# Kernel optimization log

Hardware: AMD Instinct MI355X
Metric: run time of the kernel (lower is better)

## Reference

```python
import jax, jax.numpy as jnp
import numpy as np
import math


def _lsq(x, s, bit, all_positive):
    # LSQ fake-quant: scale -> clamp -> round (STE) -> dequant
    if all_positive:
        qn, qp = 0.0, float(2 ** bit - 1)
    else:
        qn, qp = -float(2 ** (bit - 1)), float(2 ** (bit - 1) - 1)
    g = 1.0 / math.sqrt(x.size * qp)  # grad-scale factor (static)
    sg = s * g
    s_eff = sg + jax.lax.stop_gradient(s - sg)  # fwd = s, grad scaled by g
    xq = jnp.clip(x / s_eff, qn, qp)
    xq = xq + jax.lax.stop_gradient(jnp.round(xq) - xq)  # round with STE
    return xq * s_eff


def _conv(x, w, stride):
    return jax.lax.conv_general_dilated(
        x, w, window_strides=(stride, stride), padding='VALID',
        dimension_numbers=('NCHW', 'OIHW', 'NCHW'))


def setup_inputs() -> dict:
    key = jax.random.key(0)
    ks = jax.random.split(key, 5)
    B = 65536
    x = jax.random.normal(ks[0], (B, 1, 28, 28), dtype=jnp.float32)
    w1 = jax.random.normal(ks[1], (4, 1, 5, 5), dtype=jnp.float32) * 0.2
    w2 = jax.random.normal(ks[2], (8, 4, 3, 3), dtype=jnp.float32) * 0.2
    fc_w = jax.random.normal(ks[3], (10, 200), dtype=jnp.float32) * 0.07
    fc_b = jax.random.normal(ks[4], (10,), dtype=jnp.float32) * 0.01
    one = jnp.ones((1,), dtype=jnp.float32)
    return {"x": x, "w1": w1, "w2": w2, "fc_w": fc_w, "fc_b": fc_b,
            "s_in": one * 0.05, "s_w1": one * 0.02, "s_a1": one * 0.05,
            "s_w2": one * 0.02, "s_a2": one * 0.05, "s_fc": one * 0.02}


def reference(x, w1, w2, fc_w, fc_b, s_in, s_w1, s_a1, s_w2, s_a2, s_fc):
    x = _lsq(x, s_in, 8, False)
    x = _conv(x, _lsq(w1, s_w1, 8, False), 2)          # [B,4,12,12]
    x = jax.nn.relu(_lsq(x, s_a1, 8, True))
    x = _conv(x, _lsq(w2, s_w2, 8, False), 2)          # [B,8,5,5]
    x = jax.nn.relu(_lsq(x, s_a2, 8, True))
    x = x.reshape(x.shape[0], -1)                      # [B,200]
    return x @ _lsq(fc_w, s_fc, 8, False).T + fc_b     # [B,10]
```

## Files before the change

### kernel.cpp

```cpp
#include <hip/hip_runtime.h>
#include <math.h>

#define G  8
#define NG 8

#if __has_builtin(__builtin_amdgcn_sdot4)
__device__ __forceinline__ int dot4(unsigned a, unsigned b, int c) {
    return __builtin_amdgcn_sdot4((int)a, (int)b, c, false);
}
#else
__device__ __forceinline__ int dot4(unsigned a, unsigned b, int c) {
    c += (int)(signed char)(a & 255u)         * (int)(signed char)(b & 255u);
    c += (int)(signed char)((a >> 8) & 255u)  * (int)(signed char)((b >> 8) & 255u);
    c += (int)(signed char)((a >> 16) & 255u) * (int)(signed char)((b >> 16) & 255u);
    c += (int)(signed char)(a >> 24)          * (int)(signed char)(b >> 24);
    return c;
}
#endif

__device__ __forceinline__ void wave_fence() {
    asm volatile("s_waitcnt lgkmcnt(0)" ::: "memory");
}

__device__ __forceinline__ float seff(float s, float gf) {
    float sg = s * gf;
    return sg + (s - sg);
}
__device__ __forceinline__ unsigned q8(float v, float s, float rs) {
    float q0 = v * rs;
    float r  = fmaf(-s, q0, v);
    float y  = fmaf(r, rs, q0);
    y = fminf(fmaxf(y, -128.f), 127.f);
    float t = y + 12582912.0f;
    return __float_as_uint(t);
}
__device__ __forceinline__ unsigned pack4(unsigned a, unsigned b, unsigned c, unsigned d) {
    return (a & 255u) | ((b & 255u) << 8) | ((c & 255u) << 16) | (d << 24);
}
__device__ __forceinline__ int mround(int acc, double r) {
    double t = fma((double)acc, r, 6755399441055744.0);
    return (int)__double_as_longlong(t);
}


extern "C" __global__ __launch_bounds__(256, 4)
void qcnn_fused(const float* __restrict__ x,  const float* __restrict__ w1,
                const float* __restrict__ w2, const float* __restrict__ fcw,
                const float* __restrict__ fcb,
                const float* __restrict__ s_in, const float* __restrict__ s_w1,
                const float* __restrict__ s_a1, const float* __restrict__ s_w2,
                const float* __restrict__ s_a2, const float* __restrict__ s_fc,
                float* __restrict__ out, int B,
                float gx, float gw1, float ga1, float gw2, float ga2, float gfc)
{
    __shared__ __align__(16) unsigned xs[2][G*224];
    __shared__ __align__(16) unsigned a1p[2][G*144];
    __shared__ __align__(16) unsigned a2p[2][G*50];
    __shared__ __align__(16) unsigned w1pk[4][5][4];
    __shared__ unsigned w2p[8][9];
    __shared__ unsigned fcp[10][50];
    __shared__ int K2s[8];
    __shared__ int K3s[10];
    __shared__ float fcbs[10];

    const int tid = threadIdx.x;
    const int g   = tid >> 5;
    const int t   = tid & 31;

    const float sx  = seff(s_in[0], gx);
    const float sw1 = seff(s_w1[0], gw1);
    const float sa1 = seff(s_a1[0], ga1);
    const float sw2 = seff(s_w2[0], gw2);
    const float sa2 = seff(s_a2[0], ga2);
    const float sfc = seff(s_fc[0], gfc);
    const float rsx = 1.0f / sx;
    const float rw1 = 1.0f / sw1;
    const float rw2 = 1.0f / sw2;
    const float rfc = 1.0f / sfc;
    const double r1 = (double)sx  * (double)sw1 / (double)sa1;
    const double r2 = (double)sa1 * (double)sw2 / (double)sa2;
    const double r3 = (double)sa2 * (double)sfc;

    const long long gbase = (long long)blockIdx.x * NG;

    const int c8 = t & 7;
    const int eb = (t >> 3) * 7 + c8 - (c8 > 3 ? 1 : 0);

    float4 Rv0, Rv1, Rv2, Rv3, Rv4, Rv5, Rv6;
    auto stage_load = [&](long long grp) {
        const long long img = grp * G + g;
        if (img >= B) return;
        const float4* xp = (const float4*)x + img * 196;
        Rv0 = xp[eb];        Rv1 = xp[eb + 28];  Rv2 = xp[eb + 56];
        Rv3 = xp[eb + 84];   Rv4 = xp[eb + 112]; Rv5 = xp[eb + 140];
        Rv6 = xp[eb + 168];
    };
    auto stage_write = [&](long long grp, int buf) {
        const long long img = grp * G + g;
        if (img >= B) return;
        unsigned* dst = &xs[buf][g*224];
        float4 v;
        v = Rv0; dst[t]       = pack4(q8(v.x,sx,rsx), q8(v.y,sx,rsx), q8(v.z,sx,rsx), q8(v.w,sx,rsx));
        v = Rv1; dst[t + 32]  = pack4(q8(v.x,sx,rsx), q8(v.y,sx,rsx), q8(v.z,sx,rsx), q8(v.w,sx,rsx));
        v = Rv2; dst[t + 64]  = pack4(q8(v.x,sx,rsx), q8(v.y,sx,rsx), q8(v.z,sx,rsx), q8(v.w,sx,rsx));
        v = Rv3; dst[t + 96]  = pack4(q8(v.x,sx,rsx), q8(v.y,sx,rsx), q8(v.z,sx,rsx), q8(v.w,sx,rsx));
        v = Rv4; dst[t + 128] = pack4(q8(v.x,sx,rsx), q8(v.y,sx,rsx), q8(v.z,sx,rsx), q8(v.w,sx,rsx));
        v = Rv5; dst[t + 160] = pack4(q8(v.x,sx,rsx), q8(v.y,sx,rsx), q8(v.z,sx,rsx), q8(v.w,sx,rsx));
        v = Rv6; dst[t + 192] = pack4(q8(v.x,sx,rsx), q8(v.y,sx,rsx), q8(v.z,sx,rsx), q8(v.w,sx,rsx));
    };

    stage_load(gbase);

    if (tid < 80) {
        const int c = tid / 20, rem = tid % 20, ky = rem >> 2, vv = rem & 3;
        const float* wr = w1 + c*25 + ky*5;
        unsigned b[5];
        #pragma unroll
        for (int k = 0; k < 5; ++k) b[k] = q8(wr[k], sw1, rw1) & 255u;
        unsigned pk;
        if      (vv == 0) pk = b[0] | (b[1] << 8) | (b[2] << 16) | (b[3] << 24);
        else if (vv == 1) pk = b[4];
        else if (vv == 2) pk = (b[0] << 16) | (b[1] << 24);
        else              pk = b[2] | (b[3] << 8) | (b[4] << 16);
        w1pk[c][ky][vv] = pk;
    } else if (tid < 152) {
        const int d = tid - 80, oc = d / 9, tap = d % 9;
        unsigned pk = 0;
        #pragma unroll
        for (int ic = 0; ic < 4; ++ic)
            pk |= (q8(w2[oc*36 + ic*9 + tap], sw2, rw2) & 255u) << (8*ic);
        w2p[oc][tap] = pk;
    }
    if (tid < 10) fcbs[tid] = fcb[tid];
    for (int i = tid; i < 500; i += 256) {
        const int o = i / 50, kd = i % 50;
        const float* fr = fcw + o*200 + kd*4;
        fcp[o][kd] = pack4(q8(fr[0],sfc,rfc), q8(fr[1],sfc,rfc),
                           q8(fr[2],sfc,rfc), q8(fr[3],sfc,rfc));
    }
    __syncthreads();
    if (tid < 8) {
        int s = 0;
        #pragma unroll
        for (int d = 0; d < 9; ++d) s = dot4(w2p[tid][d], 0x01010101u, s);
        K2s[tid] = s << 7;
    } else if (tid < 18) {
        const int o = tid - 8;
        int s = 0;
        for (int d = 0; d < 50; ++d) s = dot4(fcp[o][d], 0x01010101u, s);
        K3s[o] = s << 7;
    }
    __syncthreads();
    stage_write(gbase, 0);
    wave_fence();

    for (int it = 0; it < NG + 2; ++it) {
        const long long grp = gbase + it;

        if (it + 1 < NG) stage_load(grp + 1);

        if (it < NG && (grp * G + g) < B) {
            const int c  = t & 3;
            const int h  = (t >> 2) & 1;
            const int y0 = t >> 3;
            uint4 W[5];
            #pragma unroll
            for (int ky = 0; ky < 5; ++ky)
                W[ky] = *(const uint4*)&w1pk[c][ky][0];
            const unsigned* xb = &xs[it & 1][g*224];
            unsigned char* a1b = (unsigned char*)&a1p[it & 1][0];
            #pragma unroll
            for (int k = 0; k < 3; ++k) {
                const int y = y0 + 4*k;
                int acc[6] = {0,0,0,0,0,0};
                #pragma unroll
                for (int ky = 0; ky < 5; ++ky) {
                    const uint4 R = *(const uint4*)&xb[(2*y + ky)*8 + 4*h];
                    acc[0] = dot4(R.y, W[ky].y, dot4(R.x, W[ky].x, acc[0]));
                    acc[1] = dot4(R.y, W[ky].w, dot4(R.x, W[ky].z, acc[1]));
                    acc[2] = dot4(R.z, W[ky].y, dot4(R.y, W[ky].x, acc[2]));
                    acc[3] = dot4(R.z, W[ky].w, dot4(R.y, W[ky].z, acc[3]));
                    acc[4] = dot4(R.w, W[ky].y, dot4(R.z, W[ky].x, acc[4]));
                    acc[5] = dot4(R.w, W[ky].w, dot4(R.z, W[ky].z, acc[5]));
                }
                unsigned char* dst = a1b + (g*144 + y*12 + 6*h)*4 + c;
                #pragma unroll
                for (int m = 0; m < 6; ++m) {
                    int q = mround(acc[m], r1);
                    q = min(max(q, 0), 255);
                    dst[4*m] = (unsigned char)(q - 128);
                }
            }
        }

        if (it >= 1 && it <= NG && ((grp - 1) * G + g) < B) {
            const int oc = t >> 2;
            unsigned wv[9];
            #pragma unroll
            for (int d = 0; d < 9; ++d) wv[d] = w2p[oc][d];
            const int k2 = K2s[oc];
            const unsigned* base = &a1p[(it - 1) & 1][g*144];
            unsigned char* dstb = (unsigned char*)&a2p[(it - 1) & 1][0] + g*200 + oc*25;
            #pragma unroll
            for (int pass = 0; pass < 2; ++pass) {
                const int y = pass ? 4 : (t & 3);
                if (pass && (t & 3) != 0) break;
                unsigned rw[3][12];
                #pragma unroll
                for (int ky = 0; ky < 3; ++ky) {
                    const uint4* rp = (const uint4*)&base[(2*y + ky)*12];
                    uint4 A = rp[0], Bv = rp[1], Cv = rp[2];
                    rw[ky][0]=A.x;  rw[ky][1]=A.y;  rw[ky][2]=A.z;  rw[ky][3]=A.w;
                    rw[ky][4]=Bv.x; rw[ky][5]=Bv.y; rw[ky][6]=Bv.z; rw[ky][7]=Bv.w;
                    rw[ky][8]=Cv.x; rw[ky][9]=Cv.y; rw[ky][10]=Cv.z; rw[ky][11]=Cv.w;
                }
                #pragma unroll
                for (int jx = 0; jx < 5; ++jx) {
                    int acc = k2;
                    #pragma unroll
                    for (int ky = 0; ky < 3; ++ky)
                        #pragma unroll
                        for (int kx = 0; kx < 3; ++kx)
                            acc = dot4(rw[ky][2*jx + kx], wv[ky*3 + kx], acc);
                    int q = mround(acc, r2);
                    q = min(max(q, 0), 255);
                    dstb[y*5 + jx] = (unsigned char)(q - 128);
                }
            }
        }

        if (it >= 2 && ((grp - 2) * G + g) < B && t < 30) {
            const int part = t / 10;
            const int o    = t - part*10;
            const int k0   = part * 17;
            const int nk   = (part == 2) ? 16 : 17;
            const unsigned* a2b = &a2p[it & 1][g*50];
            int acc = 0;
            for (int ki = 0; ki < nk; ++ki) {
                const int k = k0 + ki;
                acc = dot4(a2b[k], fcp[o][k], acc);
            }
            const int self0 = (g & 1) * 32 + o;
            const int s1 = __shfl(acc, self0 + 10);
            const int s2 = __shfl(acc, self0 + 20);
            if (part == 0) {
                const int total = acc + s1 + s2 + K3s[o];
                const double oo = (double)total * r3 + (double)fcbs[o];
                out[((grp - 2)*G + g)*10 + o] = (float)oo;
            }
        }

        if (it + 1 < NG) stage_write(grp + 1, (it + 1) & 1);

        wave_fence();
    }
}

extern "C" void kernel_launch(void* const* d_in, const int* in_sizes, int n_in,
                              void* d_out, int out_size, void* d_ws, size_t ws_size,
                              hipStream_t stream) {
    const float* x    = (const float*)d_in[0];
    const float* w1   = (const float*)d_in[1];
    const float* w2   = (const float*)d_in[2];
    const float* fcw  = (const float*)d_in[3];
    const float* fcb  = (const float*)d_in[4];
    const float* s_in = (const float*)d_in[5];
    const float* s_w1 = (const float*)d_in[6];
    const float* s_a1 = (const float*)d_in[7];
    const float* s_w2 = (const float*)d_in[8];
    const float* s_a2 = (const float*)d_in[9];
    const float* s_fc = (const float*)d_in[10];

    const int B = in_sizes[0] / 784;
    const float gx  = (float)(1.0 / sqrt((double)B * 784.0 * 127.0));
    const float gw1 = (float)(1.0 / sqrt(100.0 * 127.0));
    const float ga1 = (float)(1.0 / sqrt((double)B * 576.0 * 255.0));
    const float gw2 = (float)(1.0 / sqrt(288.0 * 127.0));
    const float ga2 = (float)(1.0 / sqrt((double)B * 200.0 * 255.0));
    const float gfc = (float)(1.0 / sqrt(2000.0 * 127.0));

    const int imgs_per_block = G * NG;
    const int grid = (B + imgs_per_block - 1) / imgs_per_block;
    qcnn_fused<<<grid, 256, 0, stream>>>(x, w1, w2, fcw, fcb,
                                         s_in, s_w1, s_a1, s_w2, s_a2, s_fc,
                                         (float*)d_out, B,
                                         gx, gw1, ga1, gw2, ga2, gfc);
}
```

Before: 55.53 us.

## Reorganize input LDS layout for row reuse in conv1 and vectorize FC dot

The quantized input tile is stored in LDS with a new row-strided layout (stride 72 per 4-row band), so each thread computes three consecutive conv1 output rows and reuses each loaded input row across overlapping kernel windows instead of reloading it per output row. The FC stage pads activations and weights to 52 words so it can use 16-byte vector LDS loads with a fixed unrolled trip count. The cost is a larger LDS footprint for the input buffer, plus more live accumulator registers in conv1, which may reduce occupancy.

```diff
diff --git a/kernel.cpp b/kernel.cpp
--- a/kernel.cpp
+++ b/kernel.cpp
@@ -53,12 +53,12 @@
                 float* __restrict__ out, int B,
                 float gx, float gw1, float ga1, float gw2, float ga2, float gfc)
 {
-    __shared__ __align__(16) unsigned xs[2][G*224];
+    __shared__ __align__(16) unsigned xs[2][G*336];
     __shared__ __align__(16) unsigned a1p[2][G*144];
-    __shared__ __align__(16) unsigned a2p[2][G*50];
+    __shared__ __align__(16) unsigned a2p[2][G*52];
     __shared__ __align__(16) unsigned w1pk[4][5][4];
     __shared__ unsigned w2p[8][9];
-    __shared__ unsigned fcp[10][50];
+    __shared__ __align__(16) unsigned fcp[10][52];
     __shared__ int K2s[8];
     __shared__ int K3s[10];
     __shared__ float fcbs[10];
@@ -85,6 +85,7 @@
 
     const int c8 = t & 7;
     const int eb = (t >> 3) * 7 + c8 - (c8 > 3 ? 1 : 0);
+    const int db = (t >> 3) * 12 + c8;
 
     float4 Rv0, Rv1, Rv2, Rv3, Rv4, Rv5, Rv6;
     auto stage_load = [&](long long grp) {
@@ -98,15 +99,15 @@
     auto stage_write = [&](long long grp, int buf) {
         const long long img = grp * G + g;
         if (img >= B) return;
-        unsigned* dst = &xs[buf][g*224];
+        unsigned* dst = &xs[buf][g*336];
         float4 v;
-        v = Rv0; dst[t]       = pack4(q8(v.x,sx,rsx), q8(v.y,sx,rsx), q8(v.z,sx,rsx), q8(v.w,sx,rsx));
-        v = Rv1; dst[t + 32]  = pack4(q8(v.x,sx,rsx), q8(v.y,sx,rsx), q8(v.z,sx,rsx), q8(v.w,sx,rsx));
-        v = Rv2; dst[t + 64]  = pack4(q8(v.x,sx,rsx), q8(v.y,sx,rsx), q8(v.z,sx,rsx), q8(v.w,sx,rsx));
-        v = Rv3; dst[t + 96]  = pack4(q8(v.x,sx,rsx), q8(v.y,sx,rsx), q8(v.z,sx,rsx), q8(v.w,sx,rsx));
-        v = Rv4; dst[t + 128] = pack4(q8(v.x,sx,rsx), q8(v.y,sx,rsx), q8(v.z,sx,rsx), q8(v.w,sx,rsx));
-        v = Rv5; dst[t + 160] = pack4(q8(v.x,sx,rsx), q8(v.y,sx,rsx), q8(v.z,sx,rsx), q8(v.w,sx,rsx));
-        v = Rv6; dst[t + 192] = pack4(q8(v.x,sx,rsx), q8(v.y,sx,rsx), q8(v.z,sx,rsx), q8(v.w,sx,rsx));
+        v = Rv0; dst[db]       = pack4(q8(v.x,sx,rsx), q8(v.y,sx,rsx), q8(v.z,sx,rsx), q8(v.w,sx,rsx));
+        v = Rv1; dst[db + 48]  = pack4(q8(v.x,sx,rsx), q8(v.y,sx,rsx), q8(v.z,sx,rsx), q8(v.w,sx,rsx));
+        v = Rv2; dst[db + 96]  = pack4(q8(v.x,sx,rsx), q8(v.y,sx,rsx), q8(v.z,sx,rsx), q8(v.w,sx,rsx));
+        v = Rv3; dst[db + 144] = pack4(q8(v.x,sx,rsx), q8(v.y,sx,rsx), q8(v.z,sx,rsx), q8(v.w,sx,rsx));
+        v = Rv4; dst[db + 192] = pack4(q8(v.x,sx,rsx), q8(v.y,sx,rsx), q8(v.z,sx,rsx), q8(v.w,sx,rsx));
+        v = Rv5; dst[db + 240] = pack4(q8(v.x,sx,rsx), q8(v.y,sx,rsx), q8(v.z,sx,rsx), q8(v.w,sx,rsx));
+        v = Rv6; dst[db + 288] = pack4(q8(v.x,sx,rsx), q8(v.y,sx,rsx), q8(v.z,sx,rsx), q8(v.w,sx,rsx));
     };
 
     stage_load(gbase);
@@ -167,30 +168,40 @@
             #pragma unroll
             for (int ky = 0; ky < 5; ++ky)
                 W[ky] = *(const uint4*)&w1pk[c][ky][0];
-            const unsigned* xb = &xs[it & 1][g*224];
+            const unsigned* xb = &xs[it & 1][g*336 + y0*72 + 4*h];
             unsigned char* a1b = (unsigned char*)&a1p[it & 1][0];
-            #pragma unroll
-            for (int k = 0; k < 3; ++k) {
-                const int y = y0 + 4*k;
-                int acc[6] = {0,0,0,0,0,0};
-                #pragma unroll
-                for (int ky = 0; ky < 5; ++ky) {
-                    const uint4 R = *(const uint4*)&xb[(2*y + ky)*8 + 4*h];
-                    acc[0] = dot4(R.y, W[ky].y, dot4(R.x, W[ky].x, acc[0]));
-                    acc[1] = dot4(R.y, W[ky].w, dot4(R.x, W[ky].z, acc[1]));
-                    acc[2] = dot4(R.z, W[ky].y, dot4(R.y, W[ky].x, acc[2]));
-                    acc[3] = dot4(R.z, W[ky].w, dot4(R.y, W[ky].z, acc[3]));
-                    acc[4] = dot4(R.w, W[ky].y, dot4(R.z, W[ky].x, acc[4]));
-                    acc[5] = dot4(R.w, W[ky].w, dot4(R.z, W[ky].z, acc[5]));
-                }
-                unsigned char* dst = a1b + (g*144 + y*12 + 6*h)*4 + c;
-                #pragma unroll
-                for (int m = 0; m < 6; ++m) {
-                    int q = mround(acc[m], r1);
-                    q = min(max(q, 0), 255);
-                    dst[4*m] = (unsigned char)(q - 128);
-                }
-            }
+            int aA[6] = {0,0,0,0,0,0};
+            int aB[6] = {0,0,0,0,0,0};
+            int aC[6] = {0,0,0,0,0,0};
+#define APPLY(A, Wk, R) \
+            A[0] = dot4(R.y, Wk.y, dot4(R.x, Wk.x, A[0])); \
+            A[1] = dot4(R.y, Wk.w, dot4(R.x, Wk.z, A[1])); \
+            A[2] = dot4(R.z, Wk.y, dot4(R.y, Wk.x, A[2])); \
+            A[3] = dot4(R.z, Wk.w, dot4(R.y, Wk.z, A[3])); \
+            A[4] = dot4(R.w, Wk.y, dot4(R.z, Wk.x, A[4])); \
+            A[5] = dot4(R.w, Wk.w, dot4(R.z, Wk.z, A[5]))
+#define EPI(A, yy) { \
+            unsigned char* dst = a1b + (g*144 + (yy)*12 + 6*h)*4 + c; \
+            _Pragma("unroll") \
+            for (int m = 0; m < 6; ++m) { \
+                int q = mround(A[m], r1); \
+                q = min(max(q, 0), 255); \
+                dst[4*m] = (unsigned char)(q - 128); } }
+            uint4 R;
+            R = *(const uint4*)&xb[0];   APPLY(aA, W[0], R);
+            R = *(const uint4*)&xb[12];  APPLY(aA, W[1], R);
+            R = *(const uint4*)&xb[24];  APPLY(aA, W[2], R); APPLY(aB, W[0], R);
+            R = *(const uint4*)&xb[36];  APPLY(aA, W[3], R); APPLY(aB, W[1], R);
+            R = *(const uint4*)&xb[48];  APPLY(aA, W[4], R); APPLY(aB, W[2], R); APPLY(aC, W[0], R);
+            EPI(aA, 3*y0);
+            R = *(const uint4*)&xb[60];  APPLY(aB, W[3], R); APPLY(aC, W[1], R);
+            R = *(const uint4*)&xb[72];  APPLY(aB, W[4], R); APPLY(aC, W[2], R);
+            EPI(aB, 3*y0 + 1);
+            R = *(const uint4*)&xb[84];  APPLY(aC, W[3], R);
+            R = *(const uint4*)&xb[96];  APPLY(aC, W[4], R);
+            EPI(aC, 3*y0 + 2);
+#undef APPLY
+#undef EPI
         }
 
         if (it >= 1 && it <= NG && ((grp - 1) * G + g) < B) {
@@ -200,7 +211,7 @@
             for (int d = 0; d < 9; ++d) wv[d] = w2p[oc][d];
             const int k2 = K2s[oc];
             const unsigned* base = &a1p[(it - 1) & 1][g*144];
-            unsigned char* dstb = (unsigned char*)&a2p[(it - 1) & 1][0] + g*200 + oc*25;
+            unsigned char* dstb = (unsigned char*)&a2p[(it - 1) & 1][0] + g*208 + oc*25;
             #pragma unroll
             for (int pass = 0; pass < 2; ++pass) {
                 const int y = pass ? 4 : (t & 3);
@@ -232,13 +243,20 @@
         if (it >= 2 && ((grp - 2) * G + g) < B && t < 30) {
             const int part = t / 10;
             const int o    = t - part*10;
-            const int k0   = part * 17;
-            const int nk   = (part == 2) ? 16 : 17;
-            const unsigned* a2b = &a2p[it & 1][g*50];
+            const int k0   = part << 4;
+            const unsigned* a2b = &a2p[it & 1][g*52];
+            const uint4* ap = (const uint4*)(a2b + k0);
+            const uint4* wp = (const uint4*)(&fcp[o][0] + k0);
             int acc = 0;
-            for (int ki = 0; ki < nk; ++ki) {
-                const int k = k0 + ki;
-                acc = dot4(a2b[k], fcp[o][k], acc);
+            #pragma unroll
+            for (int q4 = 0; q4 < 4; ++q4) {
+                uint4 a = ap[q4], w = wp[q4];
+                acc = dot4(a.x, w.x, acc); acc = dot4(a.y, w.y, acc);
+                acc = dot4(a.z, w.z, acc); acc = dot4(a.w, w.w, acc);
+            }
+            if (part == 2) {
+                acc = dot4(a2b[48], fcp[o][48], acc);
+                acc = dot4(a2b[49], fcp[o][49], acc);
             }
             const int self0 = (g & 1) * 32 + o;
             const int s1 = __shfl(acc, self0 + 10);
```

New measurement: 53.51 us, median of 2. -3.6%, faster.
